# Performance work log

Hardware: AMD Instinct MI355X
Metric: run time of the kernel (lower is better)

## Reference

```python
import jax, jax.numpy as jnp
import numpy as np

N = 50000      # nodes
E = 800000     # edges (avg degree 16)
D_IN = 128     # input_dim
H = 64         # hidden_dim (== output_dim)
L = 3          # num_layers


def setup_inputs() -> dict:
    key = jax.random.key(0)
    ks = jax.random.split(key, 24)
    s = 0.05
    p = lambda k, shape: jax.random.normal(k, shape, dtype=jnp.float32) * s
    inp = {}
    inp["node_features"] = jax.random.normal(ks[0], (N, D_IN), dtype=jnp.float32)
    inp["edge_index"] = jax.random.randint(ks[1], (2, E), 0, N, dtype=jnp.int32)
    # pre_mlp: Linear-ReLU-Linear (setup_LRL_nn with hidden_sizes=[hidden_dim])
    inp["pre_w1"] = p(ks[2], (D_IN, H)); inp["pre_b1"] = jnp.zeros((H,), jnp.float32)
    inp["pre_w2"] = p(ks[3], (H, H));    inp["pre_b2"] = jnp.zeros((H,), jnp.float32)
    # learnable skip gates (initialized to ones as in the module)
    inp["skip"] = jnp.ones((L, L), jnp.float32)
    # SAGEConv layers: lin_l (on mean-aggregated neighbors, with bias) + lin_r (root)
    for i in range(L):
        din = H * (i + 1)
        inp[f"wl{i}"] = p(ks[4 + 3 * i], (din, H))
        inp[f"bl{i}"] = jnp.zeros((H,), jnp.float32)
        inp[f"wr{i}"] = p(ks[5 + 3 * i], (din, H))
    # post_mlp: 256->64, 64->64, 64->256, 256->64
    inp["post_w1"] = p(ks[14], (H * (L + 1), H)); inp["post_b1"] = jnp.zeros((H,), jnp.float32)
    inp["post_w2"] = p(ks[15], (H, H));           inp["post_b2"] = jnp.zeros((H,), jnp.float32)
    inp["post_w3"] = p(ks[16], (H, 256));         inp["post_b3"] = jnp.zeros((256,), jnp.float32)
    inp["post_w4"] = p(ks[17], (256, H));         inp["post_b4"] = jnp.zeros((H,), jnp.float32)
    return inp


def _sage(x, src, dst, inv_deg, wl, bl, wr):
    # PyG SAGEConv (mean aggr): lin_l(mean_{j->i} x_j) + lin_r(x_i)
    agg = jax.ops.segment_sum(x[src], dst, num_segments=N) * inv_deg  # [N, Din]
    return agg @ wl + bl + x @ wr


def reference(node_features, edge_index,
              pre_w1, pre_b1, pre_w2, pre_b2, skip,
              wl0, bl0, wr0, wl1, bl1, wr1, wl2, bl2, wr2,
              post_w1, post_b1, post_w2, post_b2, post_w3, post_b3, post_w4, post_b4):
    src, dst = edge_index[0], edge_index[1]
    deg = jax.ops.segment_sum(jnp.ones((E,), jnp.float32), dst, num_segments=N)
    inv_deg = (1.0 / jnp.maximum(deg, 1.0))[:, None]  # [N,1]

    # pre_mlp
    x = jax.nn.relu(node_features @ pre_w1 + pre_b1) @ pre_w2 + pre_b2  # [N,H]

    layers = [(wl0, bl0, wr0), (wl1, bl1, wr1), (wl2, bl2, wr2)]
    all_emb = [x]
    emb = x
    for i, (wl, bl, wr) in enumerate(layers):
        gates = jax.nn.sigmoid(skip[i, :i + 1])  # [i+1]
        curr = jnp.concatenate([all_emb[j] * gates[j] for j in range(i + 1)], axis=1)  # [N, H*(i+1)]
        h = jax.nn.relu(_sage(curr, src, dst, inv_deg, wl, bl, wr))  # [N,H]  (dropout p=0)
        emb = jnp.concatenate([emb, h], axis=1)
        all_emb.append(h)

    s = jnp.sum(emb, axis=-2)  # sums over all nodes -> [H*(L+1)] (faithful to source)
    h = jax.nn.leaky_relu(s @ post_w1 + post_b1, negative_slope=0.1)
    h = jax.nn.relu(h @ post_w2 + post_b2)
    h = jax.nn.relu(h @ post_w3 + post_b3)
    return h @ post_w4 + post_b4  # [H]
```

## Files before the change

### kernel.cpp

```cpp
#include <hip/hip_runtime.h>
#include <math.h>

#define NN 50000
#define NE 800000
#define NB 196

typedef float v4f __attribute__((ext_vector_type(4)));
typedef short v8s __attribute__((ext_vector_type(8)));

__device__ __forceinline__ unsigned short f2bf(float f) {
  unsigned u = __float_as_uint(f);
  u = u + 0x7FFFu + ((u >> 16) & 1u);
  return (unsigned short)(u >> 16);
}
__device__ __forceinline__ float bf2f(unsigned short h) {
  return __uint_as_float(((unsigned)h) << 16);
}


__global__ __launch_bounds__(256) void k_bhist(const int* __restrict__ dst,
                                               int* __restrict__ gbcnt) {
  __shared__ int lcnt[NB];
  int t = threadIdx.x;
  for (int i = t; i < NB; i += 256) lcnt[i] = 0;
  __syncthreads();
  int eb = blockIdx.x * 4096;
#pragma unroll
  for (int i = 0; i < 16; ++i) {
    int e = eb + i * 256 + t;
    if (e < NE) atomicAdd(&lcnt[dst[e] >> 8], 1);
  }
  __syncthreads();
  for (int i = t; i < NB; i += 256)
    if (lcnt[i]) atomicAdd(&gbcnt[i], lcnt[i]);
}

__global__ __launch_bounds__(256) void k_bscan(const int* __restrict__ gbcnt,
                                               int* __restrict__ boff,
                                               int* __restrict__ gcur,
                                               int* __restrict__ offs) {
  __shared__ int sd[256];
  int t = threadIdx.x;
  int v = (t < NB) ? gbcnt[t] : 0;
  sd[t] = v;
  __syncthreads();
  for (int o = 1; o < 256; o <<= 1) {
    int u = (t >= o) ? sd[t - o] : 0;
    __syncthreads();
    sd[t] += u;
    __syncthreads();
  }
  if (t < NB) { int x = sd[t] - v; boff[t] = x; gcur[t] = x; }
  if (t == NB - 1) boff[NB] = sd[t];
  if (t == 0) offs[NN] = NE;
}

__global__ __launch_bounds__(256) void k_bscatter(const int* __restrict__ src,
                                                  const int* __restrict__ dst,
                                                  int* __restrict__ gcur,
                                                  unsigned* __restrict__ ebuf) {
  __shared__ int cnt[NB];
  __shared__ int base[NB];
  int t = threadIdx.x;
  for (int i = t; i < NB; i += 256) cnt[i] = 0;
  __syncthreads();
  int eb = blockIdx.x * 4096;
  unsigned pk[16];
  int bk[16], lp[16];
#pragma unroll
  for (int i = 0; i < 16; ++i) {
    int e = eb + i * 256 + t;
    if (e < NE) {
      int d = dst[e];
      int b = d >> 8;
      pk[i] = ((unsigned)src[e] << 8) | (unsigned)(d & 255);
      bk[i] = b;
      lp[i] = atomicAdd(&cnt[b], 1);
    }
  }
  __syncthreads();
  for (int i = t; i < NB; i += 256)
    base[i] = cnt[i] ? atomicAdd(&gcur[i], cnt[i]) : 0;
  __syncthreads();
#pragma unroll
  for (int i = 0; i < 16; ++i) {
    int e = eb + i * 256 + t;
    if (e < NE) ebuf[base[bk[i]] + lp[i]] = pk[i];
  }
}

__global__ __launch_bounds__(256) void k_bbuild(const unsigned* __restrict__ ebuf,
                                                const int* __restrict__ boff,
                                                int* __restrict__ offs,
                                                float* __restrict__ invd,
                                                int* __restrict__ csr) {
  __shared__ int dcnt[256];
  __shared__ int cur[256];
  int t = threadIdx.x;
  int b = blockIdx.x;
  int node0 = b << 8;
  int es = boff[b], ee = boff[b + 1];
  dcnt[t] = 0;
  __syncthreads();
  for (int e = es + t; e < ee; e += 256) atomicAdd(&dcnt[ebuf[e] & 255], 1);
  __syncthreads();
  int v = dcnt[t];
  cur[t] = v;
  __syncthreads();
  for (int o = 1; o < 256; o <<= 1) {
    int u = (t >= o) ? cur[t - o] : 0;
    __syncthreads();
    cur[t] += u;
    __syncthreads();
  }
  int excl = cur[t] - v;
  int node = node0 + t;
  if (node < NN) {
    offs[node] = es + excl;
    invd[node] = 1.0f / fmaxf((float)v, 1.0f);
  }
  __syncthreads();
  cur[t] = es + excl;
  __syncthreads();
  for (int e = es + t; e < ee; e += 256) {
    unsigned pk = ebuf[e];
    int p = atomicAdd(&cur[pk & 255], 1);
    csr[p] = (int)(pk >> 8);
  }
}

__global__ __launch_bounds__(256) void k_aggregate(
    const unsigned short* __restrict__ feat,
    const int* __restrict__ offs, const int* __restrict__ csr,
    const float* __restrict__ invd,
    unsigned short* __restrict__ mean, int n) {
  int node = blockIdx.x * 4 + (threadIdx.x >> 6);
  int lane = threadIdx.x & 63;
  int nsub = lane >> 4;
  int cg   = lane & 15;
  if (node >= n) return;
  int s = offs[node], e = offs[node + 1];

  float a[8];
#pragma unroll
  for (int i = 0; i < 8; ++i) a[i] = 0.f;

  if (e > s) {
    int emax = e - 1;
    for (int p0 = s; p0 < e; p0 += 16) {
      int pa = p0 + nsub, pb = p0 + 4 + nsub, pc = p0 + 8 + nsub, pd = p0 + 12 + nsub;
      int ja = csr[pa < emax ? pa : emax];
      int jb = csr[pb < emax ? pb : emax];
      int jc = csr[pc < emax ? pc : emax];
      int jd = csr[pd < emax ? pd : emax];
      v8s va = *(const v8s*)(feat + (size_t)ja * 128 + cg * 8);
      v8s vb = *(const v8s*)(feat + (size_t)jb * 128 + cg * 8);
      v8s vc = *(const v8s*)(feat + (size_t)jc * 128 + cg * 8);
      v8s vd = *(const v8s*)(feat + (size_t)jd * 128 + cg * 8);
      if (pa < e) {
#pragma unroll
        for (int i = 0; i < 8; ++i) a[i] += bf2f((unsigned short)va[i]);
      }
      if (pb < e) {
#pragma unroll
        for (int i = 0; i < 8; ++i) a[i] += bf2f((unsigned short)vb[i]);
      }
      if (pc < e) {
#pragma unroll
        for (int i = 0; i < 8; ++i) a[i] += bf2f((unsigned short)vc[i]);
      }
      if (pd < e) {
#pragma unroll
        for (int i = 0; i < 8; ++i) a[i] += bf2f((unsigned short)vd[i]);
      }
    }
  }
#pragma unroll
  for (int i = 0; i < 8; ++i) {
    a[i] += __shfl_xor(a[i], 8, 64);
    a[i] += __shfl_xor(a[i], 16, 64);
    a[i] += __shfl_xor(a[i], 32, 64);
  }
  if (lane < 8) {
    float d = invd[node];
    v8s oh, ol;
#pragma unroll
    for (int i = 0; i < 8; ++i) {
      float m = a[i] * d;
      unsigned short h = f2bf(m);
      oh[i] = (short)h;
      ol[i] = (short)f2bf(m - bf2f(h));
    }
    *(v8s*)(mean + (size_t)node * 128 + lane * 8) = oh;
    *(v8s*)(mean + (size_t)node * 128 + 64 + lane * 8) = ol;
  }
}

struct LinArgs {
  const void*  a[6];
  const float* w[6];
  int gidx[6];
  int stride[6];
  int isf32[6];
  int nsrc;
  const float* bias;
  const float* skip;
  unsigned short* outp;
  float* colsum;
  int n;
  int relu;
};

__global__ __launch_bounds__(256) void k_linear(LinArgs A) {
  __shared__ unsigned short sW[2][2][64 * 72];
  const int t    = threadIdx.x;
  const int lane = t & 63;
  const int wv   = t >> 6;
  const int qd   = lane >> 4;
  const int ln   = lane & 15;
  const int n0   = blockIdx.x * 64;

  v4f acc[4];
#pragma unroll
  for (int ct = 0; ct < 4; ++ct) acc[ct] = (v4f){0.f, 0.f, 0.f, 0.f};

  const int sn = t & 63;
  float wreg[16];
  auto loadW = [&](int s) {
    const float* w = A.w[s];
#pragma unroll
    for (int c = 0; c < 2; ++c) {
      int kb = (wv + 4 * c) * 8;
#pragma unroll
      for (int j = 0; j < 8; ++j)
        wreg[c * 8 + j] = w[(size_t)(kb + j) * 64 + sn];
    }
  };
  auto writeW = [&](int s, int b) {
    float gs = 1.0f;
    if (A.gidx[s] >= 0) gs = 1.0f / (1.0f + __expf(-A.skip[A.gidx[s]]));
#pragma unroll
    for (int c = 0; c < 2; ++c) {
      int cb = wv + 4 * c;
      v8s hv, lv;
#pragma unroll
      for (int j = 0; j < 8; ++j) {
        float f = wreg[c * 8 + j] * gs;
        unsigned short h = f2bf(f);
        hv[j] = (short)h;
        lv[j] = (short)f2bf(f - bf2f(h));
      }
      *(v8s*)(&sW[b][0][sn * 72 + cb * 8]) = hv;
      *(v8s*)(&sW[b][1][sn * 72 + cb * 8]) = lv;
    }
  };

  const int arow = n0 + wv * 16 + ln;
  const bool arv = arow < A.n;

  v8s rawh[2], rawl[2];
  float rawf[16];
  v8s curh[2], curl[2];
  auto loadA = [&](int s) {
    if (A.isf32[s]) {
      const float* a = (const float*)A.a[s];
      int st = A.stride[s];
      if (arv) {
#pragma unroll
        for (int ks = 0; ks < 2; ++ks) {
          const float* p = a + (size_t)arow * st + ks * 32 + qd * 8;
          float4 u0 = *(const float4*)(p);
          float4 u1 = *(const float4*)(p + 4);
          rawf[ks * 8 + 0] = u0.x; rawf[ks * 8 + 1] = u0.y;
          rawf[ks * 8 + 2] = u0.z; rawf[ks * 8 + 3] = u0.w;
          rawf[ks * 8 + 4] = u1.x; rawf[ks * 8 + 5] = u1.y;
          rawf[ks * 8 + 6] = u1.z; rawf[ks * 8 + 7] = u1.w;
        }
      } else {
#pragma unroll
        for (int j = 0; j < 16; ++j) rawf[j] = 0.f;
      }
    } else {
      const unsigned short* ph = (const unsigned short*)A.a[s] + (size_t)arow * 128;
      if (arv) {
#pragma unroll
        for (int ks = 0; ks < 2; ++ks) {
          rawh[ks] = *(const v8s*)(ph + ks * 32 + qd * 8);
          rawl[ks] = *(const v8s*)(ph + 64 + ks * 32 + qd * 8);
        }
      } else {
        v8s z;
#pragma unroll
        for (int j = 0; j < 8; ++j) z[j] = 0;
        rawh[0] = rawh[1] = rawl[0] = rawl[1] = z;
      }
    }
  };
  auto stageA = [&](int s) {
    if (A.isf32[s]) {
#pragma unroll
      for (int ks = 0; ks < 2; ++ks) {
        v8s hv, lv;
#pragma unroll
        for (int j = 0; j < 8; ++j) {
          float f = rawf[ks * 8 + j];
          unsigned short h = f2bf(f);
          hv[j] = (short)h;
          lv[j] = (short)f2bf(f - bf2f(h));
        }
        curh[ks] = hv; curl[ks] = lv;
      }
    } else {
#pragma unroll
      for (int ks = 0; ks < 2; ++ks) { curh[ks] = rawh[ks]; curl[ks] = rawl[ks]; }
    }
  };

  loadW(0);
  loadA(0);
  writeW(0, 0);
  stageA(0);
  __syncthreads();

  for (int s = 0; s < A.nsrc; ++s) {
    if (s + 1 < A.nsrc) {
      loadA(s + 1);
      loadW(s + 1);
    }
    const unsigned short* wh = &sW[s & 1][0][0];
    const unsigned short* wl = &sW[s & 1][1][0];
#pragma unroll
    for (int ks = 0; ks < 2; ++ks) {
#pragma unroll
      for (int ct = 0; ct < 4; ++ct) {
        int wn = ct * 16 + ln;
        v8s bh = *(const v8s*)(wh + wn * 72 + ks * 32 + qd * 8);
        v8s bl = *(const v8s*)(wl + wn * 72 + ks * 32 + qd * 8);
        acc[ct] = __builtin_amdgcn_mfma_f32_16x16x32_bf16(curh[ks], bh, acc[ct], 0, 0, 0);
        acc[ct] = __builtin_amdgcn_mfma_f32_16x16x32_bf16(curl[ks], bh, acc[ct], 0, 0, 0);
        acc[ct] = __builtin_amdgcn_mfma_f32_16x16x32_bf16(curh[ks], bl, acc[ct], 0, 0, 0);
      }
    }
    if (s + 1 < A.nsrc) {
      writeW(s + 1, (s + 1) & 1);
      stageA(s + 1);
    }
    __syncthreads();
  }

  float bvals[4];
#pragma unroll
  for (int ct = 0; ct < 4; ++ct) bvals[ct] = A.bias[ct * 16 + ln];

  float cs[4] = {0.f, 0.f, 0.f, 0.f};
#pragma unroll
  for (int ct = 0; ct < 4; ++ct) {
#pragma unroll
    for (int r = 0; r < 4; ++r) {
      int node = n0 + wv * 16 + qd * 4 + r;
      float v = acc[ct][r] + bvals[ct];
      if (A.relu) v = fmaxf(v, 0.f);
      if (node < A.n) {
        unsigned short h = f2bf(v);
        A.outp[(size_t)node * 128 + ct * 16 + ln] = h;
        A.outp[(size_t)node * 128 + 64 + ct * 16 + ln] = f2bf(v - bf2f(h));
        cs[ct] += v;
      }
    }
  }
  if (A.colsum) {
    float* red = (float*)&sW[0][0][0];
#pragma unroll
    for (int ct = 0; ct < 4; ++ct) {
      float v = cs[ct];
      v += __shfl_xor(v, 16, 64);
      v += __shfl_xor(v, 32, 64);
      if (qd == 0) red[wv * 64 + ct * 16 + ln] = v;
    }
    __syncthreads();
    if (t < 64) {
      float ssum = red[t] + red[64 + t] + red[128 + t] + red[192 + t];
      atomicAdd(&A.colsum[t], ssum);
    }
  }
}

__global__ __launch_bounds__(256) void k_post(const float* __restrict__ s,
                                              const float* __restrict__ w1, const float* __restrict__ b1,
                                              const float* __restrict__ w2, const float* __restrict__ b2,
                                              const float* __restrict__ w3, const float* __restrict__ b3,
                                              const float* __restrict__ w4, const float* __restrict__ b4,
                                              float* __restrict__ outp) {
  __shared__ float sh[256], h1[64], h2[64], h3[256];
  int t = threadIdx.x;
  sh[t] = s[t];
  __syncthreads();
  if (t < 64) {
    float a = b1[t];
    for (int k = 0; k < 256; ++k) a += sh[k] * w1[k * 64 + t];
    h1[t] = (a >= 0.f) ? a : 0.1f * a;
  }
  __syncthreads();
  if (t < 64) {
    float a = b2[t];
    for (int k = 0; k < 64; ++k) a += h1[k] * w2[k * 64 + t];
    h2[t] = fmaxf(a, 0.f);
  }
  __syncthreads();
  {
    float a = b3[t];
    for (int k = 0; k < 64; ++k) a += h2[k] * w3[k * 256 + t];
    h3[t] = fmaxf(a, 0.f);
  }
  __syncthreads();
  if (t < 64) {
    float a = b4[t];
    for (int k = 0; k < 256; ++k) a += h3[k] * w4[k * 64 + t];
    outp[t] = a;
  }
}

extern "C" void kernel_launch(void* const* d_in, const int* in_sizes, int n_in,
                              void* d_out, int out_size, void* d_ws, size_t ws_size,
                              hipStream_t stream) {
  const float* nf     = (const float*)d_in[0];
  const int*   ei     = (const int*)d_in[1];
  const float* pre_w1 = (const float*)d_in[2];
  const float* pre_b1 = (const float*)d_in[3];
  const float* pre_w2 = (const float*)d_in[4];
  const float* pre_b2 = (const float*)d_in[5];
  const float* skip   = (const float*)d_in[6];
  const float* wl0 = (const float*)d_in[7],  *bl0 = (const float*)d_in[8],  *wr0 = (const float*)d_in[9];
  const float* wl1 = (const float*)d_in[10], *bl1 = (const float*)d_in[11], *wr1 = (const float*)d_in[12];
  const float* wl2 = (const float*)d_in[13], *bl2 = (const float*)d_in[14], *wr2 = (const float*)d_in[15];
  const float* pw1 = (const float*)d_in[16], *pb1 = (const float*)d_in[17];
  const float* pw2 = (const float*)d_in[18], *pb2 = (const float*)d_in[19];
  const float* pw3 = (const float*)d_in[20], *pb3 = (const float*)d_in[21];
  const float* pw4 = (const float*)d_in[22], *pb4 = (const float*)d_in[23];
  float* out = (float*)d_out;

  const int N = NN, E = NE;

  char* ws = (char*)d_ws;
  size_t pos = 0;
  auto alloc = [&](size_t bytes) {
    char* p = ws + pos;
    pos += (bytes + 255) & ~(size_t)255;
    return (void*)p;
  };
  int*      gbcnt = (int*)alloc((size_t)NB * 4);
  int*      boff  = (int*)alloc((size_t)(NB + 1) * 4);
  int*      gcur  = (int*)alloc((size_t)NB * 4);
  unsigned* ebuf  = (unsigned*)alloc((size_t)E * 4);
  int*      offs  = (int*)alloc((size_t)(N + 1) * 4);
  float*    invd  = (float*)alloc((size_t)N * 4);
  int*      csr   = (int*)alloc((size_t)E * 4);
  const size_t PB = (size_t)N * 128 * 2;
  unsigned short* x  = (unsigned short*)alloc(PB);
  unsigned short* h0 = (unsigned short*)alloc(PB);
  unsigned short* h1 = (unsigned short*)alloc(PB);
  unsigned short* h2 = (unsigned short*)alloc(PB);
  unsigned short* m0 = (unsigned short*)alloc(PB);
  unsigned short* m1 = (unsigned short*)alloc(PB);
  unsigned short* m2 = (unsigned short*)alloc(PB);
  unsigned short* t0 = m2;
  float* sv = (float*)alloc(256 * 4);

  hipMemsetAsync(gbcnt, 0, (size_t)NB * 4, stream);
  hipMemsetAsync(sv, 0, 256 * 4, stream);

  const int* e_src = ei;
  const int* e_dst = ei + E;
  const int EGRID = (E + 4095) / 4096;
  k_bhist<<<EGRID, 256, 0, stream>>>(e_dst, gbcnt);
  k_bscan<<<1, 256, 0, stream>>>(gbcnt, boff, gcur, offs);
  k_bscatter<<<EGRID, 256, 0, stream>>>(e_src, e_dst, gcur, ebuf);
  k_bbuild<<<NB, 256, 0, stream>>>(ebuf, boff, offs, invd, csr);

  const int LGRID = (N + 63) / 64;
  auto lin = [&](int nsrc,
                 const void* a0, int f0, int s0, const float* w0, int g0,
                 const void* a1, int f1, int s1, const float* w1_, int g1,
                 const void* a2, int f2, int s2, const float* w2_, int g2,
                 const void* a3, int f3, int s3, const float* w3_, int g3,
                 const void* a4, int f4, int s4, const float* w4_, int g4,
                 const void* a5, int f5, int s5, const float* w5_, int g5,
                 const float* bias, unsigned short* op, float* colsum, int relu) {
    LinArgs A;
    A.a[0] = a0; A.a[1] = a1; A.a[2] = a2; A.a[3] = a3; A.a[4] = a4; A.a[5] = a5;
    A.w[0] = w0; A.w[1] = w1_; A.w[2] = w2_; A.w[3] = w3_; A.w[4] = w4_; A.w[5] = w5_;
    A.gidx[0] = g0; A.gidx[1] = g1; A.gidx[2] = g2; A.gidx[3] = g3; A.gidx[4] = g4; A.gidx[5] = g5;
    A.stride[0] = s0; A.stride[1] = s1; A.stride[2] = s2; A.stride[3] = s3; A.stride[4] = s4; A.stride[5] = s5;
    A.isf32[0] = f0; A.isf32[1] = f1; A.isf32[2] = f2; A.isf32[3] = f3; A.isf32[4] = f4; A.isf32[5] = f5;
    A.nsrc = nsrc; A.bias = bias; A.skip = skip;
    A.outp = op; A.colsum = colsum;
    A.n = N; A.relu = relu;
    k_linear<<<LGRID, 256, 0, stream>>>(A);
  };

  lin(2, nf, 1, 128, pre_w1, -1, nf + 64, 1, 128, pre_w1 + 64 * 64, -1,
      nullptr, 0, 0, nullptr, -1, nullptr, 0, 0, nullptr, -1,
      nullptr, 0, 0, nullptr, -1, nullptr, 0, 0, nullptr, -1,
      pre_b1, t0, nullptr, 1);
  lin(1, t0, 0, 0, pre_w2, -1,
      nullptr, 0, 0, nullptr, -1, nullptr, 0, 0, nullptr, -1,
      nullptr, 0, 0, nullptr, -1, nullptr, 0, 0, nullptr, -1,
      nullptr, 0, 0, nullptr, -1, pre_b2, x, sv, 0);

  k_aggregate<<<(N + 3) / 4, 256, 0, stream>>>(x, offs, csr, invd, m0, N);
  lin(2, m0, 0, 0, wl0, 0, x, 0, 0, wr0, 0,
      nullptr, 0, 0, nullptr, -1, nullptr, 0, 0, nullptr, -1,
      nullptr, 0, 0, nullptr, -1, nullptr, 0, 0, nullptr, -1,
      bl0, h0, sv + 64, 1);

  k_aggregate<<<(N + 3) / 4, 256, 0, stream>>>(h0, offs, csr, invd, m1, N);
  lin(4, m0, 0, 0, wl1, 3, m1, 0, 0, wl1 + 64 * 64, 4,
      x, 0, 0, wr1, 3, h0, 0, 0, wr1 + 64 * 64, 4,
      nullptr, 0, 0, nullptr, -1, nullptr, 0, 0, nullptr, -1,
      bl1, h1, sv + 128, 1);

  k_aggregate<<<(N + 3) / 4, 256, 0, stream>>>(h1, offs, csr, invd, m2, N);
  lin(6, m0, 0, 0, wl2, 6, m1, 0, 0, wl2 + 64 * 64, 7, m2, 0, 0, wl2 + 128 * 64, 8,
      x, 0, 0, wr2, 6, h0, 0, 0, wr2 + 64 * 64, 7, h1, 0, 0, wr2 + 128 * 64, 8,
      bl2, h2, sv + 192, 1);

  k_post<<<1, 256, 0, stream>>>(sv, pw1, pb1, pw2, pb2, pw3, pb3, pw4, pb4, out);
}
```

Before: 414.8 us.

## Precompute gated split-bf16 weights in MFMA fragment layout once, drop LDS staging

Adds a small prep kernel that applies the sigmoid skip gates to each 64x64 weight slice, splits it into hi/lo bf16, and stores it in MFMA B-fragment order. The linear kernel then reads B fragments straight from global/L2 instead of converting and staging weights in LDS per block. This removes per-block weight conversion, the LDS double buffer and the per-source __syncthreads. In exchange every wave re-reads weights from cache on each source step, and one extra kernel launch is added.

```diff
diff --git a/kernel.cpp b/kernel.cpp
--- a/kernel.cpp
+++ b/kernel.cpp
@@ -196,15 +196,48 @@
   }
 }
 
+struct WPrepArgs {
+  const float* w[15];
+  int gidx[15];
+  const float* skip;
+  unsigned short* wbuf;
+};
+
+__global__ __launch_bounds__(256) void k_wprep(WPrepArgs P) {
+  int slot = blockIdx.x;
+  int t = threadIdx.x;
+  const float* w = P.w[slot];
+  float gs = 1.0f;
+  if (P.gidx[slot] >= 0) gs = 1.0f / (1.0f + __expf(-P.skip[P.gidx[slot]]));
+  unsigned short* hi = P.wbuf + (size_t)slot * 8192;
+  unsigned short* lo = hi + 4096;
+#pragma unroll
+  for (int half = 0; half < 2; ++half) {
+    int p = t + 256 * half;
+    int frag = p >> 6, lane = p & 63;
+    int ks = frag >> 2, ct = frag & 3;
+    int qd = lane >> 4, ln = lane & 15;
+    v8s hv, lv;
+#pragma unroll
+    for (int j = 0; j < 8; ++j) {
+      float f = w[(size_t)(ks * 32 + qd * 8 + j) * 64 + ct * 16 + ln] * gs;
+      unsigned short h = f2bf(f);
+      hv[j] = (short)h;
+      lv[j] = (short)f2bf(f - bf2f(h));
+    }
+    *(v8s*)(hi + (size_t)p * 8) = hv;
+    *(v8s*)(lo + (size_t)p * 8) = lv;
+  }
+}
+
 struct LinArgs {
-  const void*  a[6];
-  const float* w[6];
-  int gidx[6];
+  const void* a[6];
+  int isf32[6];
   int stride[6];
-  int isf32[6];
+  int slot0;
   int nsrc;
   const float* bias;
-  const float* skip;
+  const unsigned short* wbuf;
   unsigned short* outp;
   float* colsum;
   int n;
@@ -212,7 +245,7 @@
 };
 
 __global__ __launch_bounds__(256) void k_linear(LinArgs A) {
-  __shared__ unsigned short sW[2][2][64 * 72];
+  __shared__ float red[256];
   const int t    = threadIdx.x;
   const int lane = t & 63;
   const int wv   = t >> 6;
@@ -223,37 +256,6 @@
   v4f acc[4];
 #pragma unroll
   for (int ct = 0; ct < 4; ++ct) acc[ct] = (v4f){0.f, 0.f, 0.f, 0.f};
-
-  const int sn = t & 63;
-  float wreg[16];
-  auto loadW = [&](int s) {
-    const float* w = A.w[s];
-#pragma unroll
-    for (int c = 0; c < 2; ++c) {
-      int kb = (wv + 4 * c) * 8;
-#pragma unroll
-      for (int j = 0; j < 8; ++j)
-        wreg[c * 8 + j] = w[(size_t)(kb + j) * 64 + sn];
-    }
-  };
-  auto writeW = [&](int s, int b) {
-    float gs = 1.0f;
-    if (A.gidx[s] >= 0) gs = 1.0f / (1.0f + __expf(-A.skip[A.gidx[s]]));
-#pragma unroll
-    for (int c = 0; c < 2; ++c) {
-      int cb = wv + 4 * c;
-      v8s hv, lv;
-#pragma unroll
-      for (int j = 0; j < 8; ++j) {
-        float f = wreg[c * 8 + j] * gs;
-        unsigned short h = f2bf(f);
-        hv[j] = (short)h;
-        lv[j] = (short)f2bf(f - bf2f(h));
-      }
-      *(v8s*)(&sW[b][0][sn * 72 + cb * 8]) = hv;
-      *(v8s*)(&sW[b][1][sn * 72 + cb * 8]) = lv;
-    }
-  };
 
   const int arow = n0 + wv * 16 + ln;
   const bool arv = arow < A.n;
@@ -316,36 +318,25 @@
     }
   };
 
-  loadW(0);
   loadA(0);
-  writeW(0, 0);
   stageA(0);
-  __syncthreads();
 
   for (int s = 0; s < A.nsrc; ++s) {
-    if (s + 1 < A.nsrc) {
-      loadA(s + 1);
-      loadW(s + 1);
-    }
-    const unsigned short* wh = &sW[s & 1][0][0];
-    const unsigned short* wl = &sW[s & 1][1][0];
+    if (s + 1 < A.nsrc) loadA(s + 1);
+    const unsigned short* wb = A.wbuf + (size_t)(A.slot0 + s) * 8192;
 #pragma unroll
     for (int ks = 0; ks < 2; ++ks) {
 #pragma unroll
       for (int ct = 0; ct < 4; ++ct) {
-        int wn = ct * 16 + ln;
-        v8s bh = *(const v8s*)(wh + wn * 72 + ks * 32 + qd * 8);
-        v8s bl = *(const v8s*)(wl + wn * 72 + ks * 32 + qd * 8);
+        const unsigned short* fp = wb + (size_t)((ks * 4 + ct) * 64 + lane) * 8;
+        v8s bh = *(const v8s*)(fp);
+        v8s bl = *(const v8s*)(fp + 4096);
         acc[ct] = __builtin_amdgcn_mfma_f32_16x16x32_bf16(curh[ks], bh, acc[ct], 0, 0, 0);
         acc[ct] = __builtin_amdgcn_mfma_f32_16x16x32_bf16(curl[ks], bh, acc[ct], 0, 0, 0);
         acc[ct] = __builtin_amdgcn_mfma_f32_16x16x32_bf16(curh[ks], bl, acc[ct], 0, 0, 0);
       }
     }
-    if (s + 1 < A.nsrc) {
-      writeW(s + 1, (s + 1) & 1);
-      stageA(s + 1);
-    }
-    __syncthreads();
+    if (s + 1 < A.nsrc) stageA(s + 1);
   }
 
   float bvals[4];
@@ -369,7 +360,6 @@
     }
   }
   if (A.colsum) {
-    float* red = (float*)&sW[0][0][0];
 #pragma unroll
     for (int ct = 0; ct < 4; ++ct) {
       float v = cs[ct];
@@ -455,6 +445,7 @@
   int*      offs  = (int*)alloc((size_t)(N + 1) * 4);
   float*    invd  = (float*)alloc((size_t)N * 4);
   int*      csr   = (int*)alloc((size_t)E * 4);
+  unsigned short* wbuf = (unsigned short*)alloc((size_t)15 * 8192 * 2);
   const size_t PB = (size_t)N * 128 * 2;
   unsigned short* x  = (unsigned short*)alloc(PB);
   unsigned short* h0 = (unsigned short*)alloc(PB);
@@ -469,6 +460,22 @@
   hipMemsetAsync(gbcnt, 0, (size_t)NB * 4, stream);
   hipMemsetAsync(sv, 0, 256 * 4, stream);
 
+  {
+    WPrepArgs P;
+    const float* wsrc[15] = {
+      pre_w1, pre_w1 + 64 * 64,
+      pre_w2,
+      wl0, wr0,
+      wl1, wl1 + 64 * 64, wr1, wr1 + 64 * 64,
+      wl2, wl2 + 64 * 64, wl2 + 128 * 64,
+      wr2, wr2 + 64 * 64, wr2 + 128 * 64
+    };
+    int gi[15] = {-1, -1, -1, 0, 0, 3, 4, 3, 4, 6, 7, 8, 6, 7, 8};
+    for (int i = 0; i < 15; ++i) { P.w[i] = wsrc[i]; P.gidx[i] = gi[i]; }
+    P.skip = skip; P.wbuf = wbuf;
+    k_wprep<<<15, 256, 0, stream>>>(P);
+  }
+
   const int* e_src = ei;
   const int* e_dst = ei + E;
   const int EGRID = (E + 4095) / 4096;
@@ -478,50 +485,43 @@
   k_bbuild<<<NB, 256, 0, stream>>>(ebuf, boff, offs, invd, csr);
 
   const int LGRID = (N + 63) / 64;
-  auto lin = [&](int nsrc,
-                 const void* a0, int f0, int s0, const float* w0, int g0,
-                 const void* a1, int f1, int s1, const float* w1_, int g1,
-                 const void* a2, int f2, int s2, const float* w2_, int g2,
-                 const void* a3, int f3, int s3, const float* w3_, int g3,
-                 const void* a4, int f4, int s4, const float* w4_, int g4,
-                 const void* a5, int f5, int s5, const float* w5_, int g5,
+  auto lin = [&](int nsrc, int slot0,
+                 const void* a0, int f0, int s0,
+                 const void* a1, int f1, int s1,
+                 const void* a2, int f2, int s2,
+                 const void* a3, int f3, int s3,
+                 const void* a4, int f4, int s4,
+                 const void* a5, int f5, int s5,
                  const float* bias, unsigned short* op, float* colsum, int relu) {
     LinArgs A;
     A.a[0] = a0; A.a[1] = a1; A.a[2] = a2; A.a[3] = a3; A.a[4] = a4; A.a[5] = a5;
-    A.w[0] = w0; A.w[1] = w1_; A.w[2] = w2_; A.w[3] = w3_; A.w[4] = w4_; A.w[5] = w5_;
-    A.gidx[0] = g0; A.gidx[1] = g1; A.gidx[2] = g2; A.gidx[3] = g3; A.gidx[4] = g4; A.gidx[5] = g5;
+    A.isf32[0] = f0; A.isf32[1] = f1; A.isf32[2] = f2; A.isf32[3] = f3; A.isf32[4] = f4; A.isf32[5] = f5;
     A.stride[0] = s0; A.stride[1] = s1; A.stride[2] = s2; A.stride[3] = s3; A.stride[4] = s4; A.stride[5] = s5;
-    A.isf32[0] = f0; A.isf32[1] = f1; A.isf32[2] = f2; A.isf32[3] = f3; A.isf32[4] = f4; A.isf32[5] = f5;
-    A.nsrc = nsrc; A.bias = bias; A.skip = skip;
+    A.slot0 = slot0; A.nsrc = nsrc; A.bias = bias; A.wbuf = wbuf;
     A.outp = op; A.colsum = colsum;
     A.n = N; A.relu = relu;
     k_linear<<<LGRID, 256, 0, stream>>>(A);
   };
 
-  lin(2, nf, 1, 128, pre_w1, -1, nf + 64, 1, 128, pre_w1 + 64 * 64, -1,
-      nullptr, 0, 0, nullptr, -1, nullptr, 0, 0, nullptr, -1,
-      nullptr, 0, 0, nullptr, -1, nullptr, 0, 0, nullptr, -1,
+  lin(2, 0, nf, 1, 128, nf + 64, 1, 128,
+      nullptr, 0, 0, nullptr, 0, 0, nullptr, 0, 0, nullptr, 0, 0,
       pre_b1, t0, nullptr, 1);
-  lin(1, t0, 0, 0, pre_w2, -1,
-      nullptr, 0, 0, nullptr, -1, nullptr, 0, 0, nullptr, -1,
-      nullptr, 0, 0, nullptr, -1, nullptr, 0, 0, nullptr, -1,
-      nullptr, 0, 0, nullptr, -1, pre_b2, x, sv, 0);
+  lin(1, 2, t0, 0, 0,
+      nullptr, 0, 0, nullptr, 0, 0, nullptr, 0, 0, nullptr, 0, 0, nullptr, 0, 0,
+      pre_b2, x, sv, 0);
 
   k_aggregate<<<(N + 3) / 4, 256, 0, stream>>>(x, offs, csr, invd, m0, N);
-  lin(2, m0, 0, 0, wl0, 0, x, 0, 0, wr0, 0,
-      nullptr, 0, 0, nullptr, -1, nullptr, 0, 0, nullptr, -1,
-      nullptr, 0, 0, nullptr, -1, nullptr, 0, 0, nullptr, -1,
+  lin(2, 3, m0, 0, 0, x, 0, 0,
+      nullptr, 0, 0, nullptr, 0, 0, nullptr, 0, 0, nullptr, 0, 0,
       bl0, h0, sv + 64, 1);
 
   k_aggregate<<<(N + 3) / 4, 256, 0, stream>>>(h0, offs, csr, invd, m1, N);
-  lin(4, m0, 0, 0, wl1, 3, m1, 0, 0, wl1 + 64 * 64, 4,
-      x, 0, 0, wr1, 3, h0, 0, 0, wr1 + 64 * 64, 4,
-      nullptr, 0, 0, nullptr, -1, nullptr, 0, 0, nullptr, -1,
+  lin(4, 5, m0, 0, 0, m1, 0, 0, x, 0, 0, h0, 0, 0,
+      nullptr, 0, 0, nullptr, 0, 0,
       bl1, h1, sv + 128, 1);
 
   k_aggregate<<<(N + 3) / 4, 256, 0, stream>>>(h1, offs, csr, invd, m2, N);
-  lin(6, m0, 0, 0, wl2, 6, m1, 0, 0, wl2 + 64 * 64, 7, m2, 0, 0, wl2 + 128 * 64, 8,
-      x, 0, 0, wr2, 6, h0, 0, 0, wr2 + 64 * 64, 7, h1, 0, 0, wr2 + 128 * 64, 8,
+  lin(6, 9, m0, 0, 0, m1, 0, 0, m2, 0, 0, x, 0, 0, h0, 0, 0, h1, 0, 0,
       bl2, h2, sv + 192, 1);
 
   k_post<<<1, 256, 0, stream>>>(sv, pw1, pb1, pw2, pb2, pw3, pb3, pw4, pb4, out);
```

New measurement: 407.7 us. About the same (-1.7%).
